# Kernel optimization log

Measured on AMD Instinct MI355X. Metric: run time of the kernel, lower is better.

## Reference

```python
import jax, jax.numpy as jnp
import numpy as np

N_NODES = 100000
N_EDGES = 1600000
IN_DIM = 128
HID = 64
OUT_DIM = 64


def setup_inputs() -> dict:
    key = jax.random.key(0)
    k = jax.random.split(key, 6)
    x = jax.random.normal(k[0], (N_NODES, IN_DIM), dtype=jnp.float32)
    edge_index = jax.random.randint(k[1], (2, N_EDGES), 0, N_NODES, dtype=jnp.int32)
    W_lin = jax.random.normal(k[2], (HID, IN_DIM), dtype=jnp.float32) * (1.0 / np.sqrt(IN_DIM))
    att = jax.random.uniform(k[3], (2 * HID,), dtype=jnp.float32, minval=-0.1, maxval=0.1)
    W_out = jax.random.normal(k[4], (OUT_DIM, HID), dtype=jnp.float32) * (1.0 / np.sqrt(HID))
    b_out = jax.random.normal(k[5], (OUT_DIM,), dtype=jnp.float32) * 0.01
    return {"x": x, "edge_index": edge_index, "W_lin": W_lin, "att": att, "W_out": W_out, "b_out": b_out}


def reference(x, edge_index, W_lin, att, W_out, b_out):
    n = x.shape[0]
    hid = W_lin.shape[0]
    h = x @ W_lin.T                                   # [N, H]
    # cat([hs,hd])*att summed == (h@a_src)[src] + (h@a_dst)[dst]
    s_node = h @ att[:hid]                            # [N]
    d_node = h @ att[hid:]                            # [N]
    src, dst = edge_index[0], edge_index[1]
    e = jax.nn.leaky_relu(s_node[src] + d_node[dst], negative_slope=0.2)  # [E]
    exp_e = jnp.exp(e - jnp.max(e))                   # global-max stabilized, as in source
    denom = jax.ops.segment_sum(exp_e, dst, num_segments=n)               # [N]
    alpha = exp_e / (denom[dst] + 1e-9)               # [E]
    msg = h[src] * alpha[:, None]                     # [E, H]
    agg = jax.ops.segment_sum(msg, dst, num_segments=n)                   # [N, H]
    z = jax.nn.relu(agg)                              # dropout is identity in eval
    return z @ W_out.T + b_out
```

## Files before the change

### kernel.cpp

```cpp
#include <hip/hip_runtime.h>

#define N_NODES 100000
#define N_EDGES 1600000
#define IN_DIM 128
#define HID 64
#define OUT_DIM 64

typedef __attribute__((ext_vector_type(8))) short short8;
typedef __attribute__((ext_vector_type(4))) float f32x4;
union FragU { short8 v; unsigned u[4]; };

__device__ __forceinline__ unsigned bf16r(float f) {
    unsigned u = __float_as_uint(f);
    return (u + 0x7FFFu + ((u >> 16) & 1u)) >> 16;
}
__device__ __forceinline__ float blo(unsigned u) { return __uint_as_float(u << 16); }
__device__ __forceinline__ float bhi(unsigned u) { return __uint_as_float(u & 0xFFFF0000u); }

#define K1_BLOCKS 1563
#define NB 391
#define CAP 4608
#define P1_BLOCKS 391
#define P1_EPB 4096

__global__ __launch_bounds__(256) void k1_p1(const float* __restrict__ x,
                                             const float* __restrict__ W,
                                             const float* __restrict__ att,
                                             uint4* __restrict__ h4,
                                             float* __restrict__ s,
                                             float* __restrict__ d,
                                             const int* __restrict__ ei,
                                             int* __restrict__ gcount,
                                             unsigned* __restrict__ ibuf) {
    __shared__ float wsL[IN_DIM], wdL[IN_DIM];
    __shared__ float scratch[4 * 64 * 17];
    const int tid = threadIdx.x;

    if (blockIdx.x >= K1_BLOCKS) {
        int* cnt  = (int*)scratch;
        int* base = cnt + NB;
        const int blk = blockIdx.x - K1_BLOCKS;
        const int e4base = blk * (P1_EPB / 4);
        for (int i = tid; i < NB; i += 256) cnt[i] = 0;
        __syncthreads();
        int pk[4][4];
#pragma unroll
        for (int c = 0; c < 4; ++c) {
            int i4 = e4base + c * 256 + tid;
            if (i4 < N_EDGES / 4) {
                int4 dv = ((const int4*)(ei + N_EDGES))[i4];
                pk[c][0] = dv.x | (atomicAdd(&cnt[dv.x >> 8], 1) << 17);
                pk[c][1] = dv.y | (atomicAdd(&cnt[dv.y >> 8], 1) << 17);
                pk[c][2] = dv.z | (atomicAdd(&cnt[dv.z >> 8], 1) << 17);
                pk[c][3] = dv.w | (atomicAdd(&cnt[dv.w >> 8], 1) << 17);
            }
        }
        __syncthreads();
        for (int b = tid; b < NB; b += 256) {
            int c = cnt[b];
            base[b] = c ? atomicAdd(&gcount[b], c) : 0;
        }
        __syncthreads();
#pragma unroll
        for (int c = 0; c < 4; ++c) {
            int i4 = e4base + c * 256 + tid;
            if (i4 < N_EDGES / 4) {
                int4 sv = ((const int4*)ei)[i4];
                int srcs[4] = {sv.x, sv.y, sv.z, sv.w};
#pragma unroll
                for (int j = 0; j < 4; ++j) {
                    unsigned p   = (unsigned)pk[c][j];
                    unsigned dst = p & 0x1FFFFu;
                    unsigned r   = p >> 17;
                    unsigned bk  = dst >> 8;
                    ibuf[bk * CAP + (unsigned)base[bk] + r] =
                        (unsigned)srcs[j] | ((dst & 255u) << 20);
                }
            }
        }
        return;
    }

    if (tid < IN_DIM) {
        float as = 0.f, ad = 0.f;
        for (int c = 0; c < HID; ++c) {
            float w = W[c * IN_DIM + tid];
            as += w * att[c];
            ad += w * att[HID + c];
        }
        wsL[tid] = as; wdL[tid] = ad;
    }
    __syncthreads();

    const int lane = tid & 63;
    const int wv = tid >> 6;
    const int l16 = lane & 15;
    const int quad = lane >> 4;
    const int tile = blockIdx.x * 4 + wv;

    FragU bfrag[4][4];
#pragma unroll
    for (int t = 0; t < 4; ++t) {
#pragma unroll
        for (int ks = 0; ks < 4; ++ks) {
            const float* wp = &W[(t * 16 + l16) * IN_DIM + ks * 32 + quad * 8];
            float4 wa = *(const float4*)wp;
            float4 wb = *(const float4*)(wp + 4);
            bfrag[t][ks].u[0] = bf16r(wa.x) | (bf16r(wa.y) << 16);
            bfrag[t][ks].u[1] = bf16r(wa.z) | (bf16r(wa.w) << 16);
            bfrag[t][ks].u[2] = bf16r(wb.x) | (bf16r(wb.y) << 16);
            bfrag[t][ks].u[3] = bf16r(wb.z) | (bf16r(wb.w) << 16);
        }
    }

    if (tile < N_NODES / 16) {
        const int rowbase = tile * 16;
        const float* xrow = &x[(size_t)(rowbase + l16) * IN_DIM];
        f32x4 acc[4] = {{0.f,0.f,0.f,0.f},{0.f,0.f,0.f,0.f},
                        {0.f,0.f,0.f,0.f},{0.f,0.f,0.f,0.f}};
        float ps = 0.f, pd = 0.f;
#pragma unroll
        for (int ks = 0; ks < 4; ++ks) {
            const int k0 = ks * 32 + quad * 8;
            float4 xa = *(const float4*)&xrow[k0];
            float4 xb = *(const float4*)&xrow[k0 + 4];
            ps += xa.x * wsL[k0]     + xa.y * wsL[k0 + 1]
                + xa.z * wsL[k0 + 2] + xa.w * wsL[k0 + 3]
                + xb.x * wsL[k0 + 4] + xb.y * wsL[k0 + 5]
                + xb.z * wsL[k0 + 6] + xb.w * wsL[k0 + 7];
            pd += xa.x * wdL[k0]     + xa.y * wdL[k0 + 1]
                + xa.z * wdL[k0 + 2] + xa.w * wdL[k0 + 3]
                + xb.x * wdL[k0 + 4] + xb.y * wdL[k0 + 5]
                + xb.z * wdL[k0 + 6] + xb.w * wdL[k0 + 7];
            FragU af;
            af.u[0] = bf16r(xa.x) | (bf16r(xa.y) << 16);
            af.u[1] = bf16r(xa.z) | (bf16r(xa.w) << 16);
            af.u[2] = bf16r(xb.x) | (bf16r(xb.y) << 16);
            af.u[3] = bf16r(xb.z) | (bf16r(xb.w) << 16);
#pragma unroll
            for (int t = 0; t < 4; ++t)
                acc[t] = __builtin_amdgcn_mfma_f32_16x16x32_bf16(
                    af.v, bfrag[t][ks].v, acc[t], 0, 0, 0);
        }
        ps += __shfl_xor(ps, 16, 64); ps += __shfl_xor(ps, 32, 64);
        pd += __shfl_xor(pd, 16, 64); pd += __shfl_xor(pd, 32, 64);
        if (quad == 0) { s[rowbase + l16] = ps; d[rowbase + l16] = pd; }
        float* sc = &scratch[wv * 64 * 17];
#pragma unroll
        for (int t = 0; t < 4; ++t)
#pragma unroll
            for (int r = 0; r < 4; ++r)
                sc[(l16 + 16 * t) * 17 + quad * 4 + r] = acc[t][r];
#pragma unroll
        for (int i = 0; i < 2; ++i) {
            int idx = i * 64 + lane;
            int nrow = idx >> 3, q = idx & 7;
            float v0 = sc[(q * 8 + 0) * 17 + nrow];
            float v1 = sc[(q * 8 + 1) * 17 + nrow];
            float v2 = sc[(q * 8 + 2) * 17 + nrow];
            float v3 = sc[(q * 8 + 3) * 17 + nrow];
            float v4 = sc[(q * 8 + 4) * 17 + nrow];
            float v5 = sc[(q * 8 + 5) * 17 + nrow];
            float v6 = sc[(q * 8 + 6) * 17 + nrow];
            float v7 = sc[(q * 8 + 7) * 17 + nrow];
            uint4 o;
            o.x = bf16r(v0) | (bf16r(v1) << 16);
            o.y = bf16r(v2) | (bf16r(v3) << 16);
            o.z = bf16r(v4) | (bf16r(v5) << 16);
            o.w = bf16r(v6) | (bf16r(v7) << 16);
            h4[(size_t)(rowbase + nrow) * 8 + q] = o;
        }
    }
}

__global__ __launch_bounds__(1024) void k_bucket2(const unsigned* __restrict__ ibuf,
                                                  const int* __restrict__ gcount,
                                                  const float* __restrict__ s,
                                                  const float* __restrict__ d,
                                                  int* __restrict__ row_start,
                                                  uint2* __restrict__ sorted) {
    __shared__ unsigned el[CAP];
    __shared__ unsigned el2[CAP];
    __shared__ unsigned short rk[CAP];
    __shared__ int cnt2[256], off2[256];
    __shared__ float dloc[256];
    __shared__ int wred[16];
    __shared__ int base_s, cnt_s;
    const int tid  = threadIdx.x;
    const int lane = tid & 63;
    const int wv   = tid >> 6;
    const int b    = blockIdx.x;

    int part = 0;
    for (int j = tid; j < b; j += 1024) part += gcount[j];
#pragma unroll
    for (int off = 32; off > 0; off >>= 1) part += __shfl_xor(part, off, 64);
    if (lane == 0) wred[wv] = part;
    if (tid < 256) {
        cnt2[tid] = 0;
        int dn = b * 256 + tid;
        dloc[tid] = (dn < N_NODES) ? d[dn] : 0.f;
    }
    __syncthreads();
    if (tid == 0) {
        int t = 0;
#pragma unroll
        for (int w = 0; w < 16; ++w) t += wred[w];
        base_s = t;
        cnt_s = gcount[b];
    }
    __syncthreads();
    const int base  = base_s;
    const int count = cnt_s;

    for (int k = tid; k < count; k += 1024) {
        unsigned v = ibuf[b * CAP + k];
        int dl = (int)(v >> 20);
        int r = atomicAdd(&cnt2[dl], 1);
        el[k] = v;
        rk[k] = (unsigned short)r;
    }
    __syncthreads();

    int v0 = 0, sc0 = 0;
    if (tid < 256) {
        v0 = cnt2[tid];
        sc0 = v0;
#pragma unroll
        for (int off = 1; off < 64; off <<= 1) {
            int t = __shfl_up(sc0, off, 64);
            if (lane >= off) sc0 += t;
        }
        if (lane == 63) wred[wv] = sc0;
    }
    __syncthreads();
    if (tid < 256) {
        int wp = 0;
#pragma unroll
        for (int w = 0; w < 4; ++w) {
            int t = wred[w];
            if (w < wv) wp += t;
        }
        int excl = wp + sc0 - v0;
        off2[tid] = excl;
        int dn = b * 256 + tid;
        if (dn < N_NODES) row_start[dn] = base + excl;
    }
    __syncthreads();

    for (int k = tid; k < count; k += 1024) {
        unsigned v = el[k];
        int dl = (int)(v >> 20);
        el2[off2[dl] + rk[k]] = v;
    }
    __syncthreads();

    for (int k = tid; k < count; k += 1024) {
        unsigned v = el2[k];
        unsigned src = v & 0xFFFFFu;
        int dl = (int)(v >> 20);
        float e = s[src] + dloc[dl];
        e = (e > 0.f) ? e : 0.2f * e;
        float ex = __expf(e);
        sorted[base + k] = make_uint2(src, __float_as_uint(ex));
    }
    if (b == NB - 1 && tid == 0) row_start[N_NODES] = base + count;
}

__global__ __launch_bounds__(256) void k3_agg(const uint2* __restrict__ sorted,
                                              const int* __restrict__ row_start,
                                              const uint4* __restrict__ h4,
                                              uint4* __restrict__ zp) {
    const int l8 = threadIdx.x & 7;
    const int node = blockIdx.x * 32 + (threadIdx.x >> 3);
    const int beg = row_start[node];
    const int end = row_start[node + 1];
    float a0 = 0.f, a1 = 0.f, a2 = 0.f, a3 = 0.f;
    float a4 = 0.f, a5 = 0.f, a6 = 0.f, a7 = 0.f, se = 0.f;
    int j = beg;
    for (; j + 3 < end; j += 4) {
        uint2 r0 = sorted[j];
        uint2 r1 = sorted[j + 1];
        uint2 r2 = sorted[j + 2];
        uint2 r3 = sorted[j + 3];
        uint4 g0 = h4[r0.x * 8u + l8];
        uint4 g1 = h4[r1.x * 8u + l8];
        uint4 g2 = h4[r2.x * 8u + l8];
        uint4 g3 = h4[r3.x * 8u + l8];
        float e0 = __uint_as_float(r0.y), e1 = __uint_as_float(r1.y);
        float e2 = __uint_as_float(r2.y), e3 = __uint_as_float(r3.y);
        se += (e0 + e1) + (e2 + e3);
        a0 += e0 * blo(g0.x) + e1 * blo(g1.x) + e2 * blo(g2.x) + e3 * blo(g3.x);
        a1 += e0 * bhi(g0.x) + e1 * bhi(g1.x) + e2 * bhi(g2.x) + e3 * bhi(g3.x);
        a2 += e0 * blo(g0.y) + e1 * blo(g1.y) + e2 * blo(g2.y) + e3 * blo(g3.y);
        a3 += e0 * bhi(g0.y) + e1 * bhi(g1.y) + e2 * bhi(g2.y) + e3 * bhi(g3.y);
        a4 += e0 * blo(g0.z) + e1 * blo(g1.z) + e2 * blo(g2.z) + e3 * blo(g3.z);
        a5 += e0 * bhi(g0.z) + e1 * bhi(g1.z) + e2 * bhi(g2.z) + e3 * bhi(g3.z);
        a6 += e0 * blo(g0.w) + e1 * blo(g1.w) + e2 * blo(g2.w) + e3 * blo(g3.w);
        a7 += e0 * bhi(g0.w) + e1 * bhi(g1.w) + e2 * bhi(g2.w) + e3 * bhi(g3.w);
    }
    for (; j < end; ++j) {
        uint2 r = sorted[j];
        uint4 g = h4[r.x * 8u + l8];
        float e = __uint_as_float(r.y);
        se += e;
        a0 += e * blo(g.x); a1 += e * bhi(g.x);
        a2 += e * blo(g.y); a3 += e * bhi(g.y);
        a4 += e * blo(g.z); a5 += e * bhi(g.z);
        a6 += e * blo(g.w); a7 += e * bhi(g.w);
    }
    float inv = 1.f / (se + 1e-9f);
    uint4 o;
    o.x = bf16r(fmaxf(a0 * inv, 0.f)) | (bf16r(fmaxf(a1 * inv, 0.f)) << 16);
    o.y = bf16r(fmaxf(a2 * inv, 0.f)) | (bf16r(fmaxf(a3 * inv, 0.f)) << 16);
    o.z = bf16r(fmaxf(a4 * inv, 0.f)) | (bf16r(fmaxf(a5 * inv, 0.f)) << 16);
    o.w = bf16r(fmaxf(a6 * inv, 0.f)) | (bf16r(fmaxf(a7 * inv, 0.f)) << 16);
    zp[node * 8 + l8] = o;
}

#define K4_M 128
#define ZPAD 133
#define WPAD4 68

__global__ __launch_bounds__(256) void k4_out(const uint2* __restrict__ zp2,
                                              const float* __restrict__ W_out,
                                              const float* __restrict__ b_out,
                                              float* __restrict__ out) {
    __shared__ float zsT[HID * ZPAD];
    __shared__ float wsT[HID * WPAD4];
    const int tid = threadIdx.x;
    const int m0g = blockIdx.x * K4_M;
    for (int i = tid; i < OUT_DIM * HID; i += 256) {
        int c = i >> 6, k = i & 63;
        wsT[k * WPAD4 + c] = W_out[i];
    }
    for (int i = tid; i < K4_M * 16; i += 256) {
        int m = i >> 4, q = i & 15;
        int row = m0g + m;
        uint2 v = (row < N_NODES) ? zp2[row * 16 + q] : make_uint2(0u, 0u);
        int kb = q * 4;
        zsT[(kb + 0) * ZPAD + m] = blo(v.x);
        zsT[(kb + 1) * ZPAD + m] = bhi(v.x);
        zsT[(kb + 2) * ZPAD + m] = blo(v.y);
        zsT[(kb + 3) * ZPAD + m] = bhi(v.y);
    }
    __syncthreads();
    const int m0 = (tid & 31) * 4;
    const int c0 = (tid >> 5) * 8;
    float acc[4][8] = {};
#pragma unroll 4
    for (int k = 0; k < HID; ++k) {
        const float4 zv = *(const float4*)&zsT[k * ZPAD + m0];
        const float4 wa = *(const float4*)&wsT[k * WPAD4 + c0];
        const float4 wb = *(const float4*)&wsT[k * WPAD4 + c0 + 4];
#pragma unroll
        for (int i2 = 0; i2 < 4; ++i2) {
            float zi = (&zv.x)[i2];
            acc[i2][0] += zi * wa.x; acc[i2][1] += zi * wa.y;
            acc[i2][2] += zi * wa.z; acc[i2][3] += zi * wa.w;
            acc[i2][4] += zi * wb.x; acc[i2][5] += zi * wb.y;
            acc[i2][6] += zi * wb.z; acc[i2][7] += zi * wb.w;
        }
    }
    const float4 b0 = *(const float4*)&b_out[c0];
    const float4 b1 = *(const float4*)&b_out[c0 + 4];
#pragma unroll
    for (int i2 = 0; i2 < 4; ++i2) {
        int row = m0g + m0 + i2;
        if (row < N_NODES) {
            *(float4*)&out[row * OUT_DIM + c0] =
                make_float4(acc[i2][0] + b0.x, acc[i2][1] + b0.y,
                            acc[i2][2] + b0.z, acc[i2][3] + b0.w);
            *(float4*)&out[row * OUT_DIM + c0 + 4] =
                make_float4(acc[i2][4] + b1.x, acc[i2][5] + b1.y,
                            acc[i2][6] + b1.z, acc[i2][7] + b1.w);
        }
    }
}

extern "C" void kernel_launch(void* const* d_in, const int* in_sizes, int n_in,
                              void* d_out, int out_size, void* d_ws, size_t ws_size,
                              hipStream_t stream) {
    const float* x     = (const float*)d_in[0];
    const int*   ei    = (const int*)d_in[1];
    const float* W_lin = (const float*)d_in[2];
    const float* att   = (const float*)d_in[3];
    const float* W_out = (const float*)d_in[4];
    const float* b_out = (const float*)d_in[5];
    float* out = (float*)d_out;

    char* ws = (char*)d_ws;
    unsigned* h2        = (unsigned*)(ws);
    float*    s         = (float*)(ws + 12800000);
    float*    d         = (float*)(ws + 13200000);
    int*      gcount    = (int*)  (ws + 13600000);
    int*      row_start = (int*)  (ws + 14000000);
    uint2*    sorted    = (uint2*)(ws + 14800016);
    unsigned* zp        = (unsigned*)(ws + 27600016);
    unsigned* ibuf      = zp;

    hipMemsetAsync(gcount, 0, NB * sizeof(int), stream);

    k1_p1<<<K1_BLOCKS + P1_BLOCKS, 256, 0, stream>>>(
        x, W_lin, att, (uint4*)h2, s, d, ei, gcount, ibuf);
    k_bucket2<<<NB, 1024, 0, stream>>>(ibuf, gcount, s, d, row_start, sorted);
    k3_agg<<<N_NODES / 32, 256, 0, stream>>>(sorted, row_start, (const uint4*)h2, (uint4*)zp);
    k4_out<<<(N_NODES + K4_M - 1) / K4_M, 256, 0, stream>>>(
        (const uint2*)zp, W_out, b_out, out);
}
```

Baseline: 211.7 us.

## Fuse bucket sort and aggregation into one kernel using LDS-resident edge lists

Merges the per-bucket counting sort and the gather/aggregate kernel, so sorted edges with their exp weights stay in shared memory instead of being written to a global sorted array and read back. This also drops the global prefix-sum over bucket counts and the row_start array. Each 1024-thread block then aggregates its 256 destination nodes directly from LDS. The cost is only 391 blocks doing the gather phase with large LDS use (about 37KB of uint2 entries), which lowers parallelism and occupancy for the latency-bound h gathers. A pragma unroll and a padding tweak are also included.

```diff
diff --git a/kernel.cpp b/kernel.cpp
--- a/kernel.cpp
+++ b/kernel.cpp
@@ -83,6 +83,7 @@
 
     if (tid < IN_DIM) {
         float as = 0.f, ad = 0.f;
+#pragma unroll
         for (int c = 0; c < HID; ++c) {
             float w = W[c * IN_DIM + tid];
             as += w * att[c];
@@ -173,52 +174,41 @@
     }
 }
 
-__global__ __launch_bounds__(1024) void k_bucket2(const unsigned* __restrict__ ibuf,
-                                                  const int* __restrict__ gcount,
-                                                  const float* __restrict__ s,
-                                                  const float* __restrict__ d,
-                                                  int* __restrict__ row_start,
-                                                  uint2* __restrict__ sorted) {
-    __shared__ unsigned el[CAP];
-    __shared__ unsigned el2[CAP];
-    __shared__ unsigned short rk[CAP];
+__global__ __launch_bounds__(1024) void k_sort_agg(const unsigned* __restrict__ ibuf,
+                                                   const int* __restrict__ gcount,
+                                                   const float* __restrict__ s,
+                                                   const float* __restrict__ d,
+                                                   const uint4* __restrict__ h4,
+                                                   uint4* __restrict__ zp) {
+    __shared__ uint2 el[CAP];
     __shared__ int cnt2[256], off2[256];
     __shared__ float dloc[256];
-    __shared__ int wred[16];
-    __shared__ int base_s, cnt_s;
+    __shared__ int wred[4];
     const int tid  = threadIdx.x;
     const int lane = tid & 63;
     const int wv   = tid >> 6;
     const int b    = blockIdx.x;
 
-    int part = 0;
-    for (int j = tid; j < b; j += 1024) part += gcount[j];
-#pragma unroll
-    for (int off = 32; off > 0; off >>= 1) part += __shfl_xor(part, off, 64);
-    if (lane == 0) wred[wv] = part;
     if (tid < 256) {
         cnt2[tid] = 0;
         int dn = b * 256 + tid;
         dloc[tid] = (dn < N_NODES) ? d[dn] : 0.f;
     }
     __syncthreads();
-    if (tid == 0) {
-        int t = 0;
-#pragma unroll
-        for (int w = 0; w < 16; ++w) t += wred[w];
-        base_s = t;
-        cnt_s = gcount[b];
-    }
-    __syncthreads();
-    const int base  = base_s;
-    const int count = cnt_s;
-
-    for (int k = tid; k < count; k += 1024) {
-        unsigned v = ibuf[b * CAP + k];
-        int dl = (int)(v >> 20);
-        int r = atomicAdd(&cnt2[dl], 1);
-        el[k] = v;
-        rk[k] = (unsigned short)r;
+    const int count = gcount[b];
+
+    unsigned vk[5];
+    int rk_[5];
+#pragma unroll
+    for (int ki = 0; ki < 5; ++ki) {
+        int k = tid + ki * 1024;
+        vk[ki] = 0u; rk_[ki] = -1;
+        if (k < count) {
+            unsigned v = ibuf[(size_t)b * CAP + k];
+            int dl = (int)(v >> 20);
+            rk_[ki] = atomicAdd(&cnt2[dl], 1);
+            vk[ki] = v;
+        }
     }
     __syncthreads();
 
@@ -241,85 +231,80 @@
             int t = wred[w];
             if (w < wv) wp += t;
         }
-        int excl = wp + sc0 - v0;
-        off2[tid] = excl;
-        int dn = b * 256 + tid;
-        if (dn < N_NODES) row_start[dn] = base + excl;
-    }
-    __syncthreads();
-
-    for (int k = tid; k < count; k += 1024) {
-        unsigned v = el[k];
-        int dl = (int)(v >> 20);
-        el2[off2[dl] + rk[k]] = v;
-    }
-    __syncthreads();
-
-    for (int k = tid; k < count; k += 1024) {
-        unsigned v = el2[k];
-        unsigned src = v & 0xFFFFFu;
-        int dl = (int)(v >> 20);
-        float e = s[src] + dloc[dl];
-        e = (e > 0.f) ? e : 0.2f * e;
-        float ex = __expf(e);
-        sorted[base + k] = make_uint2(src, __float_as_uint(ex));
-    }
-    if (b == NB - 1 && tid == 0) row_start[N_NODES] = base + count;
-}
-
-__global__ __launch_bounds__(256) void k3_agg(const uint2* __restrict__ sorted,
-                                              const int* __restrict__ row_start,
-                                              const uint4* __restrict__ h4,
-                                              uint4* __restrict__ zp) {
-    const int l8 = threadIdx.x & 7;
-    const int node = blockIdx.x * 32 + (threadIdx.x >> 3);
-    const int beg = row_start[node];
-    const int end = row_start[node + 1];
-    float a0 = 0.f, a1 = 0.f, a2 = 0.f, a3 = 0.f;
-    float a4 = 0.f, a5 = 0.f, a6 = 0.f, a7 = 0.f, se = 0.f;
-    int j = beg;
-    for (; j + 3 < end; j += 4) {
-        uint2 r0 = sorted[j];
-        uint2 r1 = sorted[j + 1];
-        uint2 r2 = sorted[j + 2];
-        uint2 r3 = sorted[j + 3];
-        uint4 g0 = h4[r0.x * 8u + l8];
-        uint4 g1 = h4[r1.x * 8u + l8];
-        uint4 g2 = h4[r2.x * 8u + l8];
-        uint4 g3 = h4[r3.x * 8u + l8];
-        float e0 = __uint_as_float(r0.y), e1 = __uint_as_float(r1.y);
-        float e2 = __uint_as_float(r2.y), e3 = __uint_as_float(r3.y);
-        se += (e0 + e1) + (e2 + e3);
-        a0 += e0 * blo(g0.x) + e1 * blo(g1.x) + e2 * blo(g2.x) + e3 * blo(g3.x);
-        a1 += e0 * bhi(g0.x) + e1 * bhi(g1.x) + e2 * bhi(g2.x) + e3 * bhi(g3.x);
-        a2 += e0 * blo(g0.y) + e1 * blo(g1.y) + e2 * blo(g2.y) + e3 * blo(g3.y);
-        a3 += e0 * bhi(g0.y) + e1 * bhi(g1.y) + e2 * bhi(g2.y) + e3 * bhi(g3.y);
-        a4 += e0 * blo(g0.z) + e1 * blo(g1.z) + e2 * blo(g2.z) + e3 * blo(g3.z);
-        a5 += e0 * bhi(g0.z) + e1 * bhi(g1.z) + e2 * bhi(g2.z) + e3 * bhi(g3.z);
-        a6 += e0 * blo(g0.w) + e1 * blo(g1.w) + e2 * blo(g2.w) + e3 * blo(g3.w);
-        a7 += e0 * bhi(g0.w) + e1 * bhi(g1.w) + e2 * bhi(g2.w) + e3 * bhi(g3.w);
-    }
-    for (; j < end; ++j) {
-        uint2 r = sorted[j];
-        uint4 g = h4[r.x * 8u + l8];
-        float e = __uint_as_float(r.y);
-        se += e;
-        a0 += e * blo(g.x); a1 += e * bhi(g.x);
-        a2 += e * blo(g.y); a3 += e * bhi(g.y);
-        a4 += e * blo(g.z); a5 += e * bhi(g.z);
-        a6 += e * blo(g.w); a7 += e * bhi(g.w);
-    }
-    float inv = 1.f / (se + 1e-9f);
-    uint4 o;
-    o.x = bf16r(fmaxf(a0 * inv, 0.f)) | (bf16r(fmaxf(a1 * inv, 0.f)) << 16);
-    o.y = bf16r(fmaxf(a2 * inv, 0.f)) | (bf16r(fmaxf(a3 * inv, 0.f)) << 16);
-    o.z = bf16r(fmaxf(a4 * inv, 0.f)) | (bf16r(fmaxf(a5 * inv, 0.f)) << 16);
-    o.w = bf16r(fmaxf(a6 * inv, 0.f)) | (bf16r(fmaxf(a7 * inv, 0.f)) << 16);
-    zp[node * 8 + l8] = o;
+        off2[tid] = wp + sc0 - v0;
+    }
+    __syncthreads();
+
+#pragma unroll
+    for (int ki = 0; ki < 5; ++ki) {
+        if (rk_[ki] >= 0) {
+            unsigned v = vk[ki];
+            unsigned src = v & 0xFFFFFu;
+            int dl = (int)(v >> 20);
+            float e = s[src] + dloc[dl];
+            e = (e > 0.f) ? e : 0.2f * e;
+            float ex = __expf(e);
+            el[off2[dl] + rk_[ki]] = make_uint2(src, __float_as_uint(ex));
+        }
+    }
+    __syncthreads();
+
+    const int l8 = tid & 7;
+    const int g = tid >> 3;
+#pragma unroll
+    for (int half = 0; half < 2; ++half) {
+        const int dl = g + half * 128;
+        const int node = b * 256 + dl;
+        if (node < N_NODES) {
+            const int o = off2[dl];
+            const int n = cnt2[dl];
+            float a0 = 0.f, a1 = 0.f, a2 = 0.f, a3 = 0.f;
+            float a4 = 0.f, a5 = 0.f, a6 = 0.f, a7 = 0.f, se = 0.f;
+            int j = 0;
+            for (; j + 3 < n; j += 4) {
+                uint2 r0 = el[o + j];
+                uint2 r1 = el[o + j + 1];
+                uint2 r2 = el[o + j + 2];
+                uint2 r3 = el[o + j + 3];
+                uint4 g0 = h4[(size_t)r0.x * 8u + l8];
+                uint4 g1 = h4[(size_t)r1.x * 8u + l8];
+                uint4 g2 = h4[(size_t)r2.x * 8u + l8];
+                uint4 g3 = h4[(size_t)r3.x * 8u + l8];
+                float e0 = __uint_as_float(r0.y), e1 = __uint_as_float(r1.y);
+                float e2 = __uint_as_float(r2.y), e3 = __uint_as_float(r3.y);
+                se += (e0 + e1) + (e2 + e3);
+                a0 += e0 * blo(g0.x) + e1 * blo(g1.x) + e2 * blo(g2.x) + e3 * blo(g3.x);
+                a1 += e0 * bhi(g0.x) + e1 * bhi(g1.x) + e2 * bhi(g2.x) + e3 * bhi(g3.x);
+                a2 += e0 * blo(g0.y) + e1 * blo(g1.y) + e2 * blo(g2.y) + e3 * blo(g3.y);
+                a3 += e0 * bhi(g0.y) + e1 * bhi(g1.y) + e2 * bhi(g2.y) + e3 * bhi(g3.y);
+                a4 += e0 * blo(g0.z) + e1 * blo(g1.z) + e2 * blo(g2.z) + e3 * blo(g3.z);
+                a5 += e0 * bhi(g0.z) + e1 * bhi(g1.z) + e2 * bhi(g2.z) + e3 * bhi(g3.z);
+                a6 += e0 * blo(g0.w) + e1 * blo(g1.w) + e2 * blo(g2.w) + e3 * blo(g3.w);
+                a7 += e0 * bhi(g0.w) + e1 * bhi(g1.w) + e2 * bhi(g2.w) + e3 * bhi(g3.w);
+            }
+            for (; j < n; ++j) {
+                uint2 r = el[o + j];
+                uint4 gg = h4[(size_t)r.x * 8u + l8];
+                float e = __uint_as_float(r.y);
+                se += e;
+                a0 += e * blo(gg.x); a1 += e * bhi(gg.x);
+                a2 += e * blo(gg.y); a3 += e * bhi(gg.y);
+                a4 += e * blo(gg.z); a5 += e * bhi(gg.z);
+                a6 += e * blo(gg.w); a7 += e * bhi(gg.w);
+            }
+            float inv = 1.f / (se + 1e-9f);
+            uint4 o4;
+            o4.x = bf16r(fmaxf(a0 * inv, 0.f)) | (bf16r(fmaxf(a1 * inv, 0.f)) << 16);
+            o4.y = bf16r(fmaxf(a2 * inv, 0.f)) | (bf16r(fmaxf(a3 * inv, 0.f)) << 16);
+            o4.z = bf16r(fmaxf(a4 * inv, 0.f)) | (bf16r(fmaxf(a5 * inv, 0.f)) << 16);
+            o4.w = bf16r(fmaxf(a6 * inv, 0.f)) | (bf16r(fmaxf(a7 * inv, 0.f)) << 16);
+            zp[(size_t)node * 8 + l8] = o4;
+        }
+    }
 }
 
 #define K4_M 128
-#define ZPAD 133
+#define ZPAD 132
 #define WPAD4 68
 
 __global__ __launch_bounds__(256) void k4_out(const uint2* __restrict__ zp2,
@@ -394,17 +379,14 @@
     float*    s         = (float*)(ws + 12800000);
     float*    d         = (float*)(ws + 13200000);
     int*      gcount    = (int*)  (ws + 13600000);
-    int*      row_start = (int*)  (ws + 14000000);
-    uint2*    sorted    = (uint2*)(ws + 14800016);
+    unsigned* ibuf      = (unsigned*)(ws + 14800016);
     unsigned* zp        = (unsigned*)(ws + 27600016);
-    unsigned* ibuf      = zp;
 
     hipMemsetAsync(gcount, 0, NB * sizeof(int), stream);
 
     k1_p1<<<K1_BLOCKS + P1_BLOCKS, 256, 0, stream>>>(
         x, W_lin, att, (uint4*)h2, s, d, ei, gcount, ibuf);
-    k_bucket2<<<NB, 1024, 0, stream>>>(ibuf, gcount, s, d, row_start, sorted);
-    k3_agg<<<N_NODES / 32, 256, 0, stream>>>(sorted, row_start, (const uint4*)h2, (uint4*)zp);
+    k_sort_agg<<<NB, 1024, 0, stream>>>(ibuf, gcount, s, d, (const uint4*)h2, (uint4*)zp);
     k4_out<<<(N_NODES + K4_M - 1) / K4_M, 256, 0, stream>>>(
         (const uint2*)zp, W_out, b_out, out);
 }
```

Result: faster. 203.9 us (-3.7%).
